# Kernel optimization log

Measured on AMD Instinct MI355X. Metric: run time of the kernel, lower is better.

The kernel has to match this reference:

```python
import jax, jax.numpy as jnp
import numpy as np

N_NODES = 50000
N_EDGES = 1600000
F_NODE, F_EDGE, HID = 16, 8, 64


def setup_inputs() -> dict:
    key = jax.random.key(0)
    ks = jax.random.split(key, 12)
    def w(k, shape):
        fan_in = shape[0]
        return jax.random.normal(k, shape, dtype=jnp.float32) / np.sqrt(fan_in)
    return {
        "x": jax.random.normal(ks[0], (N_NODES, F_NODE), dtype=jnp.float32),
        "edge_index": jax.random.randint(ks[1], (2, N_EDGES), 0, N_NODES, dtype=jnp.int32),
        "edge_attr": jax.random.normal(ks[2], (N_EDGES, F_EDGE), dtype=jnp.float32),
        "W1": w(ks[3], (F_NODE, HID)), "b1": jnp.zeros((HID,), jnp.float32),
        "W2": w(ks[4], (HID, HID)), "b2": jnp.zeros((HID,), jnp.float32),
        "mW1": w(ks[5], (2 * HID + F_EDGE, 2 * HID)), "mb1": jnp.zeros((2 * HID,), jnp.float32),
        "mW2": w(ks[6], (2 * HID, HID)), "mb2": jnp.zeros((HID,), jnp.float32),
        "mW3": w(ks[7], (HID, 1)), "mb3": jnp.zeros((1,), jnp.float32),
    }


def _gcn_conv(x, W, b, src, dst, deg_inv_sqrt, n_nodes):
    # GCNConv: D^{-1/2} (A + I) D^{-1/2} X W + b, edges include self-loops
    xw = x @ W  # [N, H]
    norm = deg_inv_sqrt[src] * deg_inv_sqrt[dst]  # [E+N]
    agg = jax.ops.segment_sum(xw[src] * norm[:, None], dst, num_segments=n_nodes)
    return agg + b


def reference(x, edge_index, edge_attr, W1, b1, W2, b2, mW1, mb1, mW2, mb2, mW3, mb3):
    n_nodes = x.shape[0]
    loop = jnp.arange(n_nodes, dtype=edge_index.dtype)
    src = jnp.concatenate([edge_index[0], loop])  # add self-loops
    dst = jnp.concatenate([edge_index[1], loop])
    deg = jax.ops.segment_sum(jnp.ones_like(dst, dtype=x.dtype), dst, num_segments=n_nodes)
    dis = jnp.where(deg > 0, jax.lax.rsqrt(deg), 0.0)

    h = jax.nn.relu(_gcn_conv(x, W1, b1, src, dst, dis, n_nodes))
    h = jax.nn.relu(_gcn_conv(h, W2, b2, src, dst, dis, n_nodes))

    # Vectorized equivalent of the per-graph neighbor loop: Q for every
    # (current_node=src, neighbor=dst) directed edge using its edge_attr.
    h_cur = h[edge_index[0]]   # [E, H]
    h_nbr = h[edge_index[1]]   # [E, H]
    z = jnp.concatenate([h_cur, h_nbr, edge_attr], axis=-1)  # [E, 2H+Fe]
    z = jax.nn.relu(z @ mW1 + mb1)
    z = jax.nn.relu(z @ mW2 + mb2)
    q = (z @ mW3 + mb3)[:, 0]  # [E]
    return q
```

## Files before the change

### kernel.cpp

```cpp
#include <hip/hip_runtime.h>
#include <hip/hip_bf16.h>

#define HID 64
#define FNODE 16
#define FEDGE 8
#define ZSTR 160

typedef __bf16 v8bf __attribute__((ext_vector_type(8)));
typedef unsigned short us8 __attribute__((ext_vector_type(8)));
typedef float v4f __attribute__((ext_vector_type(4)));

__device__ __bf16 g_w1h[20480];
__device__ __bf16 g_w1l[20480];
__device__ __bf16 g_w2h[8192];
__device__ __bf16 g_w2l[8192];

__global__ void k_pack(const float* __restrict__ mW1, const float* __restrict__ mW2) {
    int gid = blockIdx.x * 256 + threadIdx.x;
    if (gid < 20480) {
        int j = gid & 7, lane = (gid >> 3) & 63, f = gid >> 9;
        int kt = f >> 3, nt = f & 7;
        int k = kt * 32 + (lane >> 4) * 8 + j;
        int col = nt * 16 + (lane & 15);
        float x = (k < 136) ? mW1[k * 128 + col] : 0.f;
        __bf16 hi = (__bf16)x;
        g_w1h[gid] = hi;
        g_w1l[gid] = (__bf16)(x - (float)hi);
    } else if (gid < 28672) {
        int t = gid - 20480;
        int j = t & 7, lane = (t >> 3) & 63, f = t >> 9;
        int kt = f >> 2, nt = f & 3;
        int k = kt * 32 + (lane >> 4) * 8 + j;
        int col = nt * 16 + (lane & 15);
        float x = mW2[k * 64 + col];
        __bf16 hi = (__bf16)x;
        g_w2h[t] = hi;
        g_w2l[t] = (__bf16)(x - (float)hi);
    }
}

__global__ void k_count(const int* __restrict__ ei, int* __restrict__ rp, int E) {
    int e = blockIdx.x * 256 + threadIdx.x;
    if (e < E) atomicAdd(&rp[ei[E + e]], 1);
}

__global__ void k_disn(const int* __restrict__ rp, float* __restrict__ dis, int N) {
    int n = blockIdx.x * 256 + threadIdx.x;
    if (n < N) dis[n] = rsqrtf((float)(rp[n] + 1));
}

__device__ __forceinline__ int block_scan_excl(int v, int* wsum) {
    int lane = threadIdx.x & 63, wv = threadIdx.x >> 6;
    int inc = v;
#pragma unroll
    for (int d = 1; d < 64; d <<= 1) {
        int t = __shfl_up(inc, d, 64);
        if (lane >= d) inc += t;
    }
    if (lane == 63) wsum[wv] = inc;
    __syncthreads();
    int off = 0;
    for (int w = 0; w < wv; ++w) off += wsum[w];
    return off + inc - v;
}

__global__ void k_scan1(int* __restrict__ rp, int* __restrict__ bsum, int N) {
    __shared__ int ws[4];
    int i = blockIdx.x * 256 + threadIdx.x;
    int v = (i < N) ? rp[i] : 0;
    int excl = block_scan_excl(v, ws);
    if (i < N) rp[i] = excl;
    if (threadIdx.x == 255) bsum[blockIdx.x] = excl + v;
}

__global__ void k_scan2(int* __restrict__ bsum, int nb) {
    __shared__ int ws[4];
    int i = threadIdx.x;
    int v = (i < nb) ? bsum[i] : 0;
    int excl = block_scan_excl(v, ws);
    if (i < nb) bsum[i] = excl;
}

__global__ void k_scan3(int* __restrict__ rp, const int* __restrict__ bsum, int N) {
    int i = blockIdx.x * 256 + threadIdx.x;
    if (i < N) rp[i] += bsum[i >> 8];
}

__global__ void k_fill(const int* __restrict__ ei, int* __restrict__ rp,
                       int* __restrict__ ce, int* __restrict__ eid, int E) {
    int e = blockIdx.x * 256 + threadIdx.x;
    if (e < E) {
        int s = ei[e], d = ei[E + e];
        int pos = atomicAdd(&rp[d], 1);
        ce[pos] = s | (d << 16);
        eid[pos] = e;
    }
}

__global__ void k_dx(const float* __restrict__ x, const float* __restrict__ dis,
                     float* __restrict__ dx, int NF) {
    int t = blockIdx.x * 256 + threadIdx.x;
    if (t < NF) dx[t] = x[t] * dis[t >> 4];
}

__global__ __launch_bounds__(256) void k_pull1x(const float* __restrict__ dx,
                                                const int* __restrict__ rp,
                                                const int* __restrict__ ce,
                                                const float* __restrict__ dis,
                                                float* __restrict__ u, int N) {
    int grp = threadIdx.x >> 4, dim = threadIdx.x & 15;
    int n = blockIdx.x * 16 + grp;
    if (n >= N) return;
    int beg = n ? rp[n - 1] : 0;
    int end = rp[n];
    float a0 = dx[(size_t)n * 16 + dim];
    float a1 = 0.f, a2 = 0.f, a3 = 0.f;
    int j = beg;
    for (; j + 3 < end; j += 4) {
        int s0 = ce[j] & 0xffff, s1 = ce[j + 1] & 0xffff;
        int s2 = ce[j + 2] & 0xffff, s3 = ce[j + 3] & 0xffff;
        a0 += dx[(size_t)s0 * 16 + dim];
        a1 += dx[(size_t)s1 * 16 + dim];
        a2 += dx[(size_t)s2 * 16 + dim];
        a3 += dx[(size_t)s3 * 16 + dim];
    }
    for (; j < end; ++j) a0 += dx[(size_t)(ce[j] & 0xffff) * 16 + dim];
    u[(size_t)n * 16 + dim] = dis[n] * ((a0 + a1) + (a2 + a3));
}

__global__ __launch_bounds__(256) void k_h1y2(const float* __restrict__ u,
                                              const float* __restrict__ W1,
                                              const float* __restrict__ b1,
                                              const float* __restrict__ W2,
                                              const float* __restrict__ dis,
                                              float* __restrict__ y2, int N) {
    __shared__ float sh[4][64];
    int wave = threadIdx.x >> 6, lane = threadIdx.x & 63;
    int n = blockIdx.x * 4 + wave;
    if (n >= N) return;
    float myu = u[(size_t)n * 16 + (lane & 15)];
    float h = b1[lane];
#pragma unroll
    for (int k = 0; k < 16; ++k)
        h = fmaf(__shfl(myu, k, 64), W1[k * HID + lane], h);
    h = fmaxf(h, 0.f);
    sh[wave][lane] = h;
    float acc = 0.f;
#pragma unroll 8
    for (int k = 0; k < HID; ++k)
        acc = fmaf(sh[wave][k], W2[k * HID + lane], acc);
    y2[(size_t)n * HID + lane] = dis[n] * acc;
}

__global__ __launch_bounds__(256) void k_pull2(const float* __restrict__ y,
                                               const int* __restrict__ rp,
                                               const int* __restrict__ ce,
                                               const float* __restrict__ dis,
                                               const float* __restrict__ b,
                                               __bf16* __restrict__ hp, int N) {
    int wave = threadIdx.x >> 6, lane = threadIdx.x & 63;
    int n = blockIdx.x * 4 + wave;
    if (n >= N) return;
    int beg = n ? rp[n - 1] : 0;
    int end = rp[n];
    float a0 = y[(size_t)n * HID + lane];
    float a1 = 0.f, a2 = 0.f, a3 = 0.f;
    int j = beg;
    for (; j + 3 < end; j += 4) {
        int s0 = ce[j] & 0xffff, s1 = ce[j + 1] & 0xffff;
        int s2 = ce[j + 2] & 0xffff, s3 = ce[j + 3] & 0xffff;
        a0 += y[(size_t)s0 * HID + lane];
        a1 += y[(size_t)s1 * HID + lane];
        a2 += y[(size_t)s2 * HID + lane];
        a3 += y[(size_t)s3 * HID + lane];
    }
    for (; j < end; ++j) a0 += y[(size_t)(ce[j] & 0xffff) * HID + lane];
    float v = fmaxf(dis[n] * ((a0 + a1) + (a2 + a3)) + b[lane], 0.f);
    __bf16 hi = (__bf16)v;
    __bf16* p = hp + (size_t)n * 128;
    p[lane] = hi;
    p[64 + lane] = (__bf16)(v - (float)hi);
}

__global__ __launch_bounds__(256) void k_edge_mlp(
    const __bf16* __restrict__ hp, const int* __restrict__ ce,
    const int* __restrict__ eid, const float* __restrict__ ea,
    const float* __restrict__ mb1, const float* __restrict__ mb2,
    const float* __restrict__ mW3, const float* __restrict__ mb3,
    float* __restrict__ q, int E) {
    __shared__ __align__(16) __bf16 zh[64][ZSTR];
    __shared__ __align__(16) __bf16 zl[64][ZSTR];

    const int tid = threadIdx.x;
    const int lane = tid & 63;
    const int wave = tid >> 6;
    const int g = lane >> 4;
    const int cb = lane & 15;
    const int m0 = blockIdx.x * 64;

    {
        const int m = tid >> 2, qt = tid & 3;
        const int p = m0 + m;
        const bool valid = p < E;
        const int cep = valid ? ce[p] : 0;
        const int e = valid ? eid[p] : 0;
        const int s = cep & 0xffff;
        const int d = ((unsigned)cep) >> 16;
        const us8* S = (const us8*)(hp + (size_t)s * 128);
        const us8* D = (const us8*)(hp + (size_t)d * 128);
#pragma unroll
        for (int cc = 0; cc < 4; ++cc) {
            int c = qt * 4 + cc;
            us8 vs = S[c];
            us8 vd = D[c];
            __bf16* dst = (c < 8) ? &zh[m][0] : &zl[m][0];
            int base = (c & 7) * 8;
            *(us8*)&dst[base] = vs;
            *(us8*)&dst[64 + base] = vd;
        }
        if (qt < 2) {
            float buf[8];
#pragma unroll
            for (int i = 0; i < 8; ++i) buf[i] = valid ? ea[(size_t)e * FEDGE + i] : 0.f;
            __bf16* dst = qt ? &zl[m][0] : &zh[m][0];
            if (qt == 0) {
#pragma unroll
                for (int i = 0; i < 8; ++i) dst[128 + i] = (__bf16)buf[i];
            } else {
#pragma unroll
                for (int i = 0; i < 8; ++i) {
                    __bf16 h = (__bf16)buf[i];
                    dst[128 + i] = (__bf16)(buf[i] - (float)h);
                }
            }
            us8 zz = {};
#pragma unroll
            for (int c = 136; c < 160; c += 8) *(us8*)&dst[c] = zz;
        }
    }
    __syncthreads();

    const int nt0 = wave * 2;
    v4f acc[2][4];
    {
        float b0 = mb1[nt0 * 16 + cb];
        float b1v = mb1[nt0 * 16 + 16 + cb];
#pragma unroll
        for (int mt = 0; mt < 4; ++mt) {
            acc[0][mt] = (v4f){b0, b0, b0, b0};
            acc[1][mt] = (v4f){b1v, b1v, b1v, b1v};
        }
    }
    const v8bf* w1h = (const v8bf*)g_w1h;
    const v8bf* w1l = (const v8bf*)g_w1l;
#pragma unroll
    for (int kt = 0; kt < 5; ++kt) {
        v8bf bh0 = w1h[(kt * 8 + nt0) * 64 + lane];
        v8bf bl0 = w1l[(kt * 8 + nt0) * 64 + lane];
        v8bf bh1 = w1h[(kt * 8 + nt0 + 1) * 64 + lane];
        v8bf bl1 = w1l[(kt * 8 + nt0 + 1) * 64 + lane];
#pragma unroll
        for (int mt = 0; mt < 4; ++mt) {
            v8bf ah = *(const v8bf*)&zh[mt * 16 + cb][kt * 32 + g * 8];
            v8bf al = *(const v8bf*)&zl[mt * 16 + cb][kt * 32 + g * 8];
            acc[0][mt] = __builtin_amdgcn_mfma_f32_16x16x32_bf16(ah, bh0, acc[0][mt], 0, 0, 0);
            acc[0][mt] = __builtin_amdgcn_mfma_f32_16x16x32_bf16(ah, bl0, acc[0][mt], 0, 0, 0);
            acc[0][mt] = __builtin_amdgcn_mfma_f32_16x16x32_bf16(al, bh0, acc[0][mt], 0, 0, 0);
            acc[1][mt] = __builtin_amdgcn_mfma_f32_16x16x32_bf16(ah, bh1, acc[1][mt], 0, 0, 0);
            acc[1][mt] = __builtin_amdgcn_mfma_f32_16x16x32_bf16(ah, bl1, acc[1][mt], 0, 0, 0);
            acc[1][mt] = __builtin_amdgcn_mfma_f32_16x16x32_bf16(al, bh1, acc[1][mt], 0, 0, 0);
        }
    }
    __syncthreads();

#pragma unroll
    for (int c = 0; c < 2; ++c)
#pragma unroll
        for (int mt = 0; mt < 4; ++mt)
#pragma unroll
            for (int r = 0; r < 4; ++r) {
                float vv = fmaxf(acc[c][mt][r], 0.f);
                __bf16 hi = (__bf16)vv;
                int row = mt * 16 + g * 4 + r;
                int colx = (nt0 + c) * 16 + cb;
                zh[row][colx] = hi;
                zl[row][colx] = (__bf16)(vv - (float)hi);
            }
    __syncthreads();

    v4f acc2[4];
    {
        float b = mb2[wave * 16 + cb];
#pragma unroll
        for (int mt = 0; mt < 4; ++mt) acc2[mt] = (v4f){b, b, b, b};
    }
    const v8bf* w2h = (const v8bf*)g_w2h;
    const v8bf* w2l = (const v8bf*)g_w2l;
#pragma unroll
    for (int kt = 0; kt < 4; ++kt) {
        v8bf bh = w2h[(kt * 4 + wave) * 64 + lane];
        v8bf bl = w2l[(kt * 4 + wave) * 64 + lane];
#pragma unroll
        for (int mt = 0; mt < 4; ++mt) {
            v8bf ah = *(const v8bf*)&zh[mt * 16 + cb][kt * 32 + g * 8];
            v8bf al = *(const v8bf*)&zl[mt * 16 + cb][kt * 32 + g * 8];
            acc2[mt] = __builtin_amdgcn_mfma_f32_16x16x32_bf16(ah, bh, acc2[mt], 0, 0, 0);
            acc2[mt] = __builtin_amdgcn_mfma_f32_16x16x32_bf16(ah, bl, acc2[mt], 0, 0, 0);
            acc2[mt] = __builtin_amdgcn_mfma_f32_16x16x32_bf16(al, bh, acc2[mt], 0, 0, 0);
        }
    }
    __syncthreads();

    float* qp = (float*)&zh[0][0];
    const float w3 = mW3[wave * 16 + cb];
#pragma unroll
    for (int mt = 0; mt < 4; ++mt) {
#pragma unroll
        for (int r = 0; r < 4; ++r) {
            float pr = fmaxf(acc2[mt][r], 0.f) * w3;
            pr += __shfl_xor(pr, 1, 16);
            pr += __shfl_xor(pr, 2, 16);
            pr += __shfl_xor(pr, 4, 16);
            pr += __shfl_xor(pr, 8, 16);
            if (cb == 0) qp[wave * 64 + mt * 16 + g * 4 + r] = pr;
        }
    }
    __syncthreads();
    if (tid < 64) {
        int p = m0 + tid;
        if (p < E)
            q[eid[p]] = qp[tid] + qp[64 + tid] + qp[128 + tid] + qp[192 + tid] +
                        mb3[0];
    }
}

extern "C" void kernel_launch(void* const* d_in, const int* in_sizes, int n_in,
                              void* d_out, int out_size, void* d_ws, size_t ws_size,
                              hipStream_t stream) {
    const float* x   = (const float*)d_in[0];
    const int*   ei  = (const int*)d_in[1];
    const float* ea  = (const float*)d_in[2];
    const float* W1  = (const float*)d_in[3];
    const float* b1  = (const float*)d_in[4];
    const float* W2  = (const float*)d_in[5];
    const float* b2  = (const float*)d_in[6];
    const float* mW1 = (const float*)d_in[7];
    const float* mb1 = (const float*)d_in[8];
    const float* mW2 = (const float*)d_in[9];
    const float* mb2 = (const float*)d_in[10];
    const float* mW3 = (const float*)d_in[11];
    const float* mb3 = (const float*)d_in[12];
    float* q = (float*)d_out;

    const int N = in_sizes[0] / FNODE;
    const int E = in_sizes[1] / 2;

    float* dis = (float*)d_ws;
    int* bsum  = (int*)(dis + 50000);
    float* y2  = dis + ((N + 511) & ~255);
    float* hpf = y2 + (size_t)N * HID;
    float* dx  = hpf;
    float* u   = hpf + (size_t)N * 16;
    int* rp    = (int*)(hpf + (size_t)N * HID);
    int* ce    = rp + ((N + 255) & ~255);
    int* eid   = ce + E;

    const int nT = 256;
    const int gN    = (N + nT - 1) / nT;
    const int gE    = (E + nT - 1) / nT;
    const int gNF   = (N * FNODE + nT - 1) / nT;
    const int g16   = (N + 15) / 16;
    const int gNode = (N + 3) / 4;
    const int gMLP  = (E + 63) / 64;

    k_pack<<<112, nT, 0, stream>>>(mW1, mW2);

    hipMemsetAsync(rp, 0, (size_t)N * sizeof(int), stream);
    k_count<<<gE, nT, 0, stream>>>(ei, rp, E);
    k_disn<<<gN, nT, 0, stream>>>(rp, dis, N);
    k_scan1<<<gN, nT, 0, stream>>>(rp, bsum, N);
    k_scan2<<<1, nT, 0, stream>>>(bsum, gN);
    k_scan3<<<gN, nT, 0, stream>>>(rp, bsum, N);
    k_fill<<<gE, nT, 0, stream>>>(ei, rp, ce, eid, E);

    k_dx<<<gNF, nT, 0, stream>>>(x, dis, dx, N * FNODE);
    k_pull1x<<<g16, nT, 0, stream>>>(dx, rp, ce, dis, u, N);
    k_h1y2<<<gNode, nT, 0, stream>>>(u, W1, b1, W2, dis, y2, N);

    k_pull2<<<gNode, nT, 0, stream>>>(y2, rp, ce, dis, b2, (__bf16*)hpf, N);

    k_edge_mlp<<<gMLP, nT, 0, stream>>>((const __bf16*)hpf, ce, eid, ea, mb1, mb2,
                                        mW3, mb3, q, E);
}
```

Measured before the change: 757.3 us.

## Make edge MLP persistent with register-prefetched next tile; unroll gathers by eight

Turns the edge MLP kernel into a persistent grid-stride loop over 64-edge tiles on 1024 blocks. While the current tile is in the MFMA phases, the next tile's node features and edge attributes are gathered into registers to hide gather latency. The two GCN pull kernels also unroll their neighbor loops to eight independent accumulators for more loads in flight. The trade-off is higher register pressure from the prefetch buffers under the (256,4) launch bound, and a fixed grid size that may not match the device well.

```diff
diff --git a/kernel.cpp b/kernel.cpp
--- a/kernel.cpp
+++ b/kernel.cpp
@@ -114,18 +114,21 @@
     int beg = n ? rp[n - 1] : 0;
     int end = rp[n];
     float a0 = dx[(size_t)n * 16 + dim];
-    float a1 = 0.f, a2 = 0.f, a3 = 0.f;
+    float a1 = 0.f, a2 = 0.f, a3 = 0.f, a4 = 0.f, a5 = 0.f, a6 = 0.f, a7 = 0.f;
     int j = beg;
-    for (; j + 3 < end; j += 4) {
-        int s0 = ce[j] & 0xffff, s1 = ce[j + 1] & 0xffff;
-        int s2 = ce[j + 2] & 0xffff, s3 = ce[j + 3] & 0xffff;
-        a0 += dx[(size_t)s0 * 16 + dim];
-        a1 += dx[(size_t)s1 * 16 + dim];
-        a2 += dx[(size_t)s2 * 16 + dim];
-        a3 += dx[(size_t)s3 * 16 + dim];
+    for (; j + 7 < end; j += 8) {
+        a0 += dx[(size_t)(ce[j] & 0xffff) * 16 + dim];
+        a1 += dx[(size_t)(ce[j + 1] & 0xffff) * 16 + dim];
+        a2 += dx[(size_t)(ce[j + 2] & 0xffff) * 16 + dim];
+        a3 += dx[(size_t)(ce[j + 3] & 0xffff) * 16 + dim];
+        a4 += dx[(size_t)(ce[j + 4] & 0xffff) * 16 + dim];
+        a5 += dx[(size_t)(ce[j + 5] & 0xffff) * 16 + dim];
+        a6 += dx[(size_t)(ce[j + 6] & 0xffff) * 16 + dim];
+        a7 += dx[(size_t)(ce[j + 7] & 0xffff) * 16 + dim];
     }
     for (; j < end; ++j) a0 += dx[(size_t)(ce[j] & 0xffff) * 16 + dim];
-    u[(size_t)n * 16 + dim] = dis[n] * ((a0 + a1) + (a2 + a3));
+    u[(size_t)n * 16 + dim] =
+        dis[n] * (((a0 + a1) + (a2 + a3)) + ((a4 + a5) + (a6 + a7)));
 }
 
 __global__ __launch_bounds__(256) void k_h1y2(const float* __restrict__ u,
@@ -164,30 +167,39 @@
     int beg = n ? rp[n - 1] : 0;
     int end = rp[n];
     float a0 = y[(size_t)n * HID + lane];
-    float a1 = 0.f, a2 = 0.f, a3 = 0.f;
+    float a1 = 0.f, a2 = 0.f, a3 = 0.f, a4 = 0.f, a5 = 0.f, a6 = 0.f, a7 = 0.f;
     int j = beg;
-    for (; j + 3 < end; j += 4) {
-        int s0 = ce[j] & 0xffff, s1 = ce[j + 1] & 0xffff;
-        int s2 = ce[j + 2] & 0xffff, s3 = ce[j + 3] & 0xffff;
-        a0 += y[(size_t)s0 * HID + lane];
-        a1 += y[(size_t)s1 * HID + lane];
-        a2 += y[(size_t)s2 * HID + lane];
-        a3 += y[(size_t)s3 * HID + lane];
+    for (; j + 7 < end; j += 8) {
+        a0 += y[(size_t)(ce[j] & 0xffff) * HID + lane];
+        a1 += y[(size_t)(ce[j + 1] & 0xffff) * HID + lane];
+        a2 += y[(size_t)(ce[j + 2] & 0xffff) * HID + lane];
+        a3 += y[(size_t)(ce[j + 3] & 0xffff) * HID + lane];
+        a4 += y[(size_t)(ce[j + 4] & 0xffff) * HID + lane];
+        a5 += y[(size_t)(ce[j + 5] & 0xffff) * HID + lane];
+        a6 += y[(size_t)(ce[j + 6] & 0xffff) * HID + lane];
+        a7 += y[(size_t)(ce[j + 7] & 0xffff) * HID + lane];
     }
     for (; j < end; ++j) a0 += y[(size_t)(ce[j] & 0xffff) * HID + lane];
-    float v = fmaxf(dis[n] * ((a0 + a1) + (a2 + a3)) + b[lane], 0.f);
+    float v = fmaxf(
+        dis[n] * (((a0 + a1) + (a2 + a3)) + ((a4 + a5) + (a6 + a7))) + b[lane], 0.f);
     __bf16 hi = (__bf16)v;
     __bf16* p = hp + (size_t)n * 128;
     p[lane] = hi;
     p[64 + lane] = (__bf16)(v - (float)hi);
 }
 
-__global__ __launch_bounds__(256) void k_edge_mlp(
+struct ETile {
+    us8 s0, s1, s2, s3;
+    us8 d0, d1, d2, d3;
+    float4 ea;
+};
+
+__global__ __launch_bounds__(256, 4) void k_edge_mlp(
     const __bf16* __restrict__ hp, const int* __restrict__ ce,
     const int* __restrict__ eid, const float* __restrict__ ea,
     const float* __restrict__ mb1, const float* __restrict__ mb2,
     const float* __restrict__ mW3, const float* __restrict__ mb3,
-    float* __restrict__ q, int E) {
+    float* __restrict__ q, int E, int nTiles) {
     __shared__ __align__(16) __bf16 zh[64][ZSTR];
     __shared__ __align__(16) __bf16 zl[64][ZSTR];
 
@@ -196,141 +208,167 @@
     const int wave = tid >> 6;
     const int g = lane >> 4;
     const int cb = lane & 15;
-    const int m0 = blockIdx.x * 64;
-
-    {
-        const int m = tid >> 2, qt = tid & 3;
-        const int p = m0 + m;
-        const bool valid = p < E;
-        const int cep = valid ? ce[p] : 0;
-        const int e = valid ? eid[p] : 0;
-        const int s = cep & 0xffff;
-        const int d = ((unsigned)cep) >> 16;
-        const us8* S = (const us8*)(hp + (size_t)s * 128);
-        const us8* D = (const us8*)(hp + (size_t)d * 128);
-#pragma unroll
-        for (int cc = 0; cc < 4; ++cc) {
-            int c = qt * 4 + cc;
-            us8 vs = S[c];
-            us8 vd = D[c];
-            __bf16* dst = (c < 8) ? &zh[m][0] : &zl[m][0];
-            int base = (c & 7) * 8;
-            *(us8*)&dst[base] = vs;
-            *(us8*)&dst[64 + base] = vd;
-        }
-        if (qt < 2) {
-            float buf[8];
-#pragma unroll
-            for (int i = 0; i < 8; ++i) buf[i] = valid ? ea[(size_t)e * FEDGE + i] : 0.f;
-            __bf16* dst = qt ? &zl[m][0] : &zh[m][0];
-            if (qt == 0) {
-#pragma unroll
-                for (int i = 0; i < 8; ++i) dst[128 + i] = (__bf16)buf[i];
-            } else {
-#pragma unroll
-                for (int i = 0; i < 8; ++i) {
-                    __bf16 h = (__bf16)buf[i];
-                    dst[128 + i] = (__bf16)(buf[i] - (float)h);
-                }
-            }
-            us8 zz = {};
-#pragma unroll
-            for (int c = 136; c < 160; c += 8) *(us8*)&dst[c] = zz;
-        }
-    }
-    __syncthreads();
-
-    const int nt0 = wave * 2;
-    v4f acc[2][4];
-    {
-        float b0 = mb1[nt0 * 16 + cb];
-        float b1v = mb1[nt0 * 16 + 16 + cb];
-#pragma unroll
-        for (int mt = 0; mt < 4; ++mt) {
-            acc[0][mt] = (v4f){b0, b0, b0, b0};
-            acc[1][mt] = (v4f){b1v, b1v, b1v, b1v};
-        }
-    }
+    const int m = tid >> 2, qt = tid & 3;
+    const int stride = gridDim.x;
+
     const v8bf* w1h = (const v8bf*)g_w1h;
     const v8bf* w1l = (const v8bf*)g_w1l;
-#pragma unroll
-    for (int kt = 0; kt < 5; ++kt) {
-        v8bf bh0 = w1h[(kt * 8 + nt0) * 64 + lane];
-        v8bf bl0 = w1l[(kt * 8 + nt0) * 64 + lane];
-        v8bf bh1 = w1h[(kt * 8 + nt0 + 1) * 64 + lane];
-        v8bf bl1 = w1l[(kt * 8 + nt0 + 1) * 64 + lane];
-#pragma unroll
-        for (int mt = 0; mt < 4; ++mt) {
-            v8bf ah = *(const v8bf*)&zh[mt * 16 + cb][kt * 32 + g * 8];
-            v8bf al = *(const v8bf*)&zl[mt * 16 + cb][kt * 32 + g * 8];
-            acc[0][mt] = __builtin_amdgcn_mfma_f32_16x16x32_bf16(ah, bh0, acc[0][mt], 0, 0, 0);
-            acc[0][mt] = __builtin_amdgcn_mfma_f32_16x16x32_bf16(ah, bl0, acc[0][mt], 0, 0, 0);
-            acc[0][mt] = __builtin_amdgcn_mfma_f32_16x16x32_bf16(al, bh0, acc[0][mt], 0, 0, 0);
-            acc[1][mt] = __builtin_amdgcn_mfma_f32_16x16x32_bf16(ah, bh1, acc[1][mt], 0, 0, 0);
-            acc[1][mt] = __builtin_amdgcn_mfma_f32_16x16x32_bf16(ah, bl1, acc[1][mt], 0, 0, 0);
-            acc[1][mt] = __builtin_amdgcn_mfma_f32_16x16x32_bf16(al, bh1, acc[1][mt], 0, 0, 0);
-        }
-    }
-    __syncthreads();
-
-#pragma unroll
-    for (int c = 0; c < 2; ++c)
-#pragma unroll
-        for (int mt = 0; mt < 4; ++mt)
-#pragma unroll
-            for (int r = 0; r < 4; ++r) {
-                float vv = fmaxf(acc[c][mt][r], 0.f);
-                __bf16 hi = (__bf16)vv;
-                int row = mt * 16 + g * 4 + r;
-                int colx = (nt0 + c) * 16 + cb;
-                zh[row][colx] = hi;
-                zl[row][colx] = (__bf16)(vv - (float)hi);
-            }
-    __syncthreads();
-
-    v4f acc2[4];
-    {
-        float b = mb2[wave * 16 + cb];
-#pragma unroll
-        for (int mt = 0; mt < 4; ++mt) acc2[mt] = (v4f){b, b, b, b};
-    }
     const v8bf* w2h = (const v8bf*)g_w2h;
     const v8bf* w2l = (const v8bf*)g_w2l;
-#pragma unroll
-    for (int kt = 0; kt < 4; ++kt) {
-        v8bf bh = w2h[(kt * 4 + wave) * 64 + lane];
-        v8bf bl = w2l[(kt * 4 + wave) * 64 + lane];
+    const int nt0 = wave * 2;
+
+    auto prefetch = [&](int t, ETile& T) {
+        int p = t * 64 + m;
+        bool valid = p < E;
+        int cep = valid ? ce[p] : 0;
+        int s = cep & 0xffff;
+        int d = ((unsigned)cep) >> 16;
+        const us8* S = (const us8*)(hp + (size_t)s * 128) + qt * 4;
+        const us8* D = (const us8*)(hp + (size_t)d * 128) + qt * 4;
+        T.s0 = S[0]; T.s1 = S[1]; T.s2 = S[2]; T.s3 = S[3];
+        T.d0 = D[0]; T.d1 = D[1]; T.d2 = D[2]; T.d3 = D[3];
+        if (qt < 2) {
+            if (valid) {
+                int e = eid[p];
+                T.ea = *(const float4*)(ea + (size_t)e * FEDGE + qt * 4);
+            } else {
+                T.ea = (float4){0.f, 0.f, 0.f, 0.f};
+            }
+        }
+    };
+
+    auto stage = [&](const ETile& T) {
+#define PUTC(cc, VS, VD)                                     \
+    {                                                        \
+        int c = qt * 4 + cc;                                 \
+        __bf16* dst = (c < 8) ? &zh[m][0] : &zl[m][0];       \
+        int base = (c & 7) * 8;                              \
+        *(us8*)&dst[base] = VS;                              \
+        *(us8*)&dst[64 + base] = VD;                         \
+    }
+        PUTC(0, T.s0, T.d0)
+        PUTC(1, T.s1, T.d1)
+        PUTC(2, T.s2, T.d2)
+        PUTC(3, T.s3, T.d3)
+#undef PUTC
+        if (qt < 2) {
+            int base = 128 + qt * 4;
+#define PUTEA(i, V)                                  \
+    {                                                \
+        __bf16 hiv = (__bf16)(V);                    \
+        zh[m][base + i] = hiv;                       \
+        zl[m][base + i] = (__bf16)((V) - (float)hiv);\
+    }
+            PUTEA(0, T.ea.x) PUTEA(1, T.ea.y) PUTEA(2, T.ea.z) PUTEA(3, T.ea.w)
+#undef PUTEA
+        } else {
+            __bf16* dst = (qt == 2) ? &zh[m][136] : &zl[m][136];
+            us8 zz = {};
+            *(us8*)&dst[0] = zz;
+            *(us8*)&dst[8] = zz;
+            *(us8*)&dst[16] = zz;
+        }
+    };
+
+    ETile A, B;
+    int t = blockIdx.x;
+    if (t < nTiles) prefetch(t, A);
+
+    for (; t < nTiles; t += stride) {
+        __syncthreads();
+        stage(A);
+        int tn = t + stride;
+        if (tn < nTiles) prefetch(tn, B);
+        __syncthreads();
+
+        v4f acc[2][4];
+        {
+            float b0 = mb1[nt0 * 16 + cb];
+            float b1v = mb1[nt0 * 16 + 16 + cb];
+#pragma unroll
+            for (int mt = 0; mt < 4; ++mt) {
+                acc[0][mt] = (v4f){b0, b0, b0, b0};
+                acc[1][mt] = (v4f){b1v, b1v, b1v, b1v};
+            }
+        }
+#pragma unroll
+        for (int kt = 0; kt < 5; ++kt) {
+            v8bf bh0 = w1h[(kt * 8 + nt0) * 64 + lane];
+            v8bf bl0 = w1l[(kt * 8 + nt0) * 64 + lane];
+            v8bf bh1 = w1h[(kt * 8 + nt0 + 1) * 64 + lane];
+            v8bf bl1 = w1l[(kt * 8 + nt0 + 1) * 64 + lane];
+#pragma unroll
+            for (int mt = 0; mt < 4; ++mt) {
+                v8bf ah = *(const v8bf*)&zh[mt * 16 + cb][kt * 32 + g * 8];
+                v8bf al = *(const v8bf*)&zl[mt * 16 + cb][kt * 32 + g * 8];
+                acc[0][mt] = __builtin_amdgcn_mfma_f32_16x16x32_bf16(ah, bh0, acc[0][mt], 0, 0, 0);
+                acc[0][mt] = __builtin_amdgcn_mfma_f32_16x16x32_bf16(ah, bl0, acc[0][mt], 0, 0, 0);
+                acc[0][mt] = __builtin_amdgcn_mfma_f32_16x16x32_bf16(al, bh0, acc[0][mt], 0, 0, 0);
+                acc[1][mt] = __builtin_amdgcn_mfma_f32_16x16x32_bf16(ah, bh1, acc[1][mt], 0, 0, 0);
+                acc[1][mt] = __builtin_amdgcn_mfma_f32_16x16x32_bf16(ah, bl1, acc[1][mt], 0, 0, 0);
+                acc[1][mt] = __builtin_amdgcn_mfma_f32_16x16x32_bf16(al, bh1, acc[1][mt], 0, 0, 0);
+            }
+        }
+        __syncthreads();
+
+#pragma unroll
+        for (int c = 0; c < 2; ++c)
+#pragma unroll
+            for (int mt = 0; mt < 4; ++mt)
+#pragma unroll
+                for (int r = 0; r < 4; ++r) {
+                    float vv = fmaxf(acc[c][mt][r], 0.f);
+                    __bf16 hi = (__bf16)vv;
+                    int row = mt * 16 + g * 4 + r;
+                    int colx = (nt0 + c) * 16 + cb;
+                    zh[row][colx] = hi;
+                    zl[row][colx] = (__bf16)(vv - (float)hi);
+                }
+        __syncthreads();
+
+        v4f acc2[4];
+        {
+            float b = mb2[wave * 16 + cb];
+#pragma unroll
+            for (int mt = 0; mt < 4; ++mt) acc2[mt] = (v4f){b, b, b, b};
+        }
+#pragma unroll
+        for (int kt = 0; kt < 4; ++kt) {
+            v8bf bh = w2h[(kt * 4 + wave) * 64 + lane];
+            v8bf bl = w2l[(kt * 4 + wave) * 64 + lane];
+#pragma unroll
+            for (int mt = 0; mt < 4; ++mt) {
+                v8bf ah = *(const v8bf*)&zh[mt * 16 + cb][kt * 32 + g * 8];
+                v8bf al = *(const v8bf*)&zl[mt * 16 + cb][kt * 32 + g * 8];
+                acc2[mt] = __builtin_amdgcn_mfma_f32_16x16x32_bf16(ah, bh, acc2[mt], 0, 0, 0);
+                acc2[mt] = __builtin_amdgcn_mfma_f32_16x16x32_bf16(ah, bl, acc2[mt], 0, 0, 0);
+                acc2[mt] = __builtin_amdgcn_mfma_f32_16x16x32_bf16(al, bh, acc2[mt], 0, 0, 0);
+            }
+        }
+        __syncthreads();
+
+        float* qp = (float*)&zh[0][0];
+        const float w3 = mW3[wave * 16 + cb];
 #pragma unroll
         for (int mt = 0; mt < 4; ++mt) {
-            v8bf ah = *(const v8bf*)&zh[mt * 16 + cb][kt * 32 + g * 8];
-            v8bf al = *(const v8bf*)&zl[mt * 16 + cb][kt * 32 + g * 8];
-            acc2[mt] = __builtin_amdgcn_mfma_f32_16x16x32_bf16(ah, bh, acc2[mt], 0, 0, 0);
-            acc2[mt] = __builtin_amdgcn_mfma_f32_16x16x32_bf16(ah, bl, acc2[mt], 0, 0, 0);
-            acc2[mt] = __builtin_amdgcn_mfma_f32_16x16x32_bf16(al, bh, acc2[mt], 0, 0, 0);
-        }
-    }
-    __syncthreads();
-
-    float* qp = (float*)&zh[0][0];
-    const float w3 = mW3[wave * 16 + cb];
-#pragma unroll
-    for (int mt = 0; mt < 4; ++mt) {
-#pragma unroll
-        for (int r = 0; r < 4; ++r) {
-            float pr = fmaxf(acc2[mt][r], 0.f) * w3;
-            pr += __shfl_xor(pr, 1, 16);
-            pr += __shfl_xor(pr, 2, 16);
-            pr += __shfl_xor(pr, 4, 16);
-            pr += __shfl_xor(pr, 8, 16);
-            if (cb == 0) qp[wave * 64 + mt * 16 + g * 4 + r] = pr;
-        }
-    }
-    __syncthreads();
-    if (tid < 64) {
-        int p = m0 + tid;
-        if (p < E)
-            q[eid[p]] = qp[tid] + qp[64 + tid] + qp[128 + tid] + qp[192 + tid] +
-                        mb3[0];
+#pragma unroll
+            for (int r = 0; r < 4; ++r) {
+                float pr = fmaxf(acc2[mt][r], 0.f) * w3;
+                pr += __shfl_xor(pr, 1, 16);
+                pr += __shfl_xor(pr, 2, 16);
+                pr += __shfl_xor(pr, 4, 16);
+                pr += __shfl_xor(pr, 8, 16);
+                if (cb == 0) qp[wave * 64 + mt * 16 + g * 4 + r] = pr;
+            }
+        }
+        __syncthreads();
+        if (tid < 64) {
+            int p = t * 64 + tid;
+            if (p < E)
+                q[eid[p]] =
+                    qp[tid] + qp[64 + tid] + qp[128 + tid] + qp[192 + tid] + mb3[0];
+        }
+        A = B;
     }
 }
 
@@ -371,7 +409,7 @@
     const int gNF   = (N * FNODE + nT - 1) / nT;
     const int g16   = (N + 15) / 16;
     const int gNode = (N + 3) / 4;
-    const int gMLP  = (E + 63) / 64;
+    const int nTiles = (E + 63) / 64;
 
     k_pack<<<112, nT, 0, stream>>>(mW1, mW2);
 
@@ -389,6 +427,6 @@
 
     k_pull2<<<gNode, nT, 0, stream>>>(y2, rp, ce, dis, b2, (__bf16*)hpf, N);
 
-    k_edge_mlp<<<gMLP, nT, 0, stream>>>((const __bf16*)hpf, ce, eid, ea, mb1, mb2,
-                                        mW3, mb3, q, E);
-}
+    k_edge_mlp<<<1024, nT, 0, stream>>>((const __bf16*)hpf, ce, eid, ea, mb1, mb2,
+                                        mW3, mb3, q, E, nTiles);
+}
```

Result: slower. 951.5 us (+25.6%).

## Gather node features straight to LDS and retile edge-MLP staging layout

Applied to the files above, without the earlier changes.

The edge MLP now gathers the source and destination node rows with global_load_lds (direct global-to-LDS DMA) into a new tiled LDS layout given by zoff. Edge attributes go into separate small hi/lo buffers loaded as float4. The goal is to skip the register round trip and cut LDS bank conflicts in the A-operand reads. The two pull kernels also unroll the neighbour gather from 4 to 8 accumulators for more memory-level parallelism. This adds complex layout indexing and relies on the exact byte layout of the LDS DMA, where a mismatch would corrupt data.

```diff
diff --git a/kernel.cpp b/kernel.cpp
--- a/kernel.cpp
+++ b/kernel.cpp
@@ -4,7 +4,6 @@
 #define HID 64
 #define FNODE 16
 #define FEDGE 8
-#define ZSTR 160
 
 typedef __bf16 v8bf __attribute__((ext_vector_type(8)));
 typedef unsigned short us8 __attribute__((ext_vector_type(8)));
@@ -114,18 +113,21 @@
     int beg = n ? rp[n - 1] : 0;
     int end = rp[n];
     float a0 = dx[(size_t)n * 16 + dim];
-    float a1 = 0.f, a2 = 0.f, a3 = 0.f;
+    float a1 = 0.f, a2 = 0.f, a3 = 0.f, a4 = 0.f, a5 = 0.f, a6 = 0.f, a7 = 0.f;
     int j = beg;
-    for (; j + 3 < end; j += 4) {
-        int s0 = ce[j] & 0xffff, s1 = ce[j + 1] & 0xffff;
-        int s2 = ce[j + 2] & 0xffff, s3 = ce[j + 3] & 0xffff;
-        a0 += dx[(size_t)s0 * 16 + dim];
-        a1 += dx[(size_t)s1 * 16 + dim];
-        a2 += dx[(size_t)s2 * 16 + dim];
-        a3 += dx[(size_t)s3 * 16 + dim];
+    for (; j + 7 < end; j += 8) {
+        a0 += dx[(size_t)(ce[j] & 0xffff) * 16 + dim];
+        a1 += dx[(size_t)(ce[j + 1] & 0xffff) * 16 + dim];
+        a2 += dx[(size_t)(ce[j + 2] & 0xffff) * 16 + dim];
+        a3 += dx[(size_t)(ce[j + 3] & 0xffff) * 16 + dim];
+        a4 += dx[(size_t)(ce[j + 4] & 0xffff) * 16 + dim];
+        a5 += dx[(size_t)(ce[j + 5] & 0xffff) * 16 + dim];
+        a6 += dx[(size_t)(ce[j + 6] & 0xffff) * 16 + dim];
+        a7 += dx[(size_t)(ce[j + 7] & 0xffff) * 16 + dim];
     }
     for (; j < end; ++j) a0 += dx[(size_t)(ce[j] & 0xffff) * 16 + dim];
-    u[(size_t)n * 16 + dim] = dis[n] * ((a0 + a1) + (a2 + a3));
+    u[(size_t)n * 16 + dim] =
+        dis[n] * (((a0 + a1) + (a2 + a3)) + ((a4 + a5) + (a6 + a7)));
 }
 
 __global__ __launch_bounds__(256) void k_h1y2(const float* __restrict__ u,
@@ -164,22 +166,29 @@
     int beg = n ? rp[n - 1] : 0;
     int end = rp[n];
     float a0 = y[(size_t)n * HID + lane];
-    float a1 = 0.f, a2 = 0.f, a3 = 0.f;
+    float a1 = 0.f, a2 = 0.f, a3 = 0.f, a4 = 0.f, a5 = 0.f, a6 = 0.f, a7 = 0.f;
     int j = beg;
-    for (; j + 3 < end; j += 4) {
-        int s0 = ce[j] & 0xffff, s1 = ce[j + 1] & 0xffff;
-        int s2 = ce[j + 2] & 0xffff, s3 = ce[j + 3] & 0xffff;
-        a0 += y[(size_t)s0 * HID + lane];
-        a1 += y[(size_t)s1 * HID + lane];
-        a2 += y[(size_t)s2 * HID + lane];
-        a3 += y[(size_t)s3 * HID + lane];
+    for (; j + 7 < end; j += 8) {
+        a0 += y[(size_t)(ce[j] & 0xffff) * HID + lane];
+        a1 += y[(size_t)(ce[j + 1] & 0xffff) * HID + lane];
+        a2 += y[(size_t)(ce[j + 2] & 0xffff) * HID + lane];
+        a3 += y[(size_t)(ce[j + 3] & 0xffff) * HID + lane];
+        a4 += y[(size_t)(ce[j + 4] & 0xffff) * HID + lane];
+        a5 += y[(size_t)(ce[j + 5] & 0xffff) * HID + lane];
+        a6 += y[(size_t)(ce[j + 6] & 0xffff) * HID + lane];
+        a7 += y[(size_t)(ce[j + 7] & 0xffff) * HID + lane];
     }
     for (; j < end; ++j) a0 += y[(size_t)(ce[j] & 0xffff) * HID + lane];
-    float v = fmaxf(dis[n] * ((a0 + a1) + (a2 + a3)) + b[lane], 0.f);
+    float v = fmaxf(
+        dis[n] * (((a0 + a1) + (a2 + a3)) + ((a4 + a5) + (a6 + a7))) + b[lane], 0.f);
     __bf16 hi = (__bf16)v;
     __bf16* p = hp + (size_t)n * 128;
     p[lane] = hi;
     p[64 + lane] = (__bf16)(v - (float)hi);
+}
+
+__device__ __forceinline__ int zoff(int m, int ch) {
+    return ((m >> 4) << 12) + ((ch >> 2) << 9) + ((m & 15) << 5) + ((ch & 3) << 3);
 }
 
 __global__ __launch_bounds__(256) void k_edge_mlp(
@@ -188,8 +197,9 @@
     const float* __restrict__ mb1, const float* __restrict__ mb2,
     const float* __restrict__ mW3, const float* __restrict__ mb3,
     float* __restrict__ q, int E) {
-    __shared__ __align__(16) __bf16 zh[64][ZSTR];
-    __shared__ __align__(16) __bf16 zl[64][ZSTR];
+    __shared__ __align__(16) __bf16 zc[16384];
+    __shared__ __align__(16) __bf16 eh[64][32];
+    __shared__ __align__(16) __bf16 el[64][32];
 
     const int tid = threadIdx.x;
     const int lane = tid & 63;
@@ -199,43 +209,53 @@
     const int m0 = blockIdx.x * 64;
 
     {
+        const int me = wave * 16 + (lane >> 2);
+        const int cl = lane & 3;
+        const int p = m0 + me;
+        const bool valid = p < E;
+        const int cep = valid ? ce[p] : 0;
+        const int s = cep & 0xffff;
+        const int d = ((unsigned)cep) >> 16;
+        const __bf16* Sp = hp + (size_t)s * 128 + cl * 8;
+        const __bf16* Dp = hp + (size_t)d * 128 + cl * 8;
+        __bf16* lb = zc + wave * 4096;
+#pragma unroll
+        for (int i = 0; i < 4; ++i)
+            __builtin_amdgcn_global_load_lds(
+                (const __attribute__((address_space(1))) unsigned int*)(Sp + i * 32),
+                (__attribute__((address_space(3))) unsigned int*)(lb + i * 512),
+                16, 0, 0);
+#pragma unroll
+        for (int i = 0; i < 4; ++i)
+            __builtin_amdgcn_global_load_lds(
+                (const __attribute__((address_space(1))) unsigned int*)(Dp + i * 32),
+                (__attribute__((address_space(3))) unsigned int*)(lb + (4 + i) * 512),
+                16, 0, 0);
+    }
+    {
         const int m = tid >> 2, qt = tid & 3;
         const int p = m0 + m;
         const bool valid = p < E;
-        const int cep = valid ? ce[p] : 0;
-        const int e = valid ? eid[p] : 0;
-        const int s = cep & 0xffff;
-        const int d = ((unsigned)cep) >> 16;
-        const us8* S = (const us8*)(hp + (size_t)s * 128);
-        const us8* D = (const us8*)(hp + (size_t)d * 128);
-#pragma unroll
-        for (int cc = 0; cc < 4; ++cc) {
-            int c = qt * 4 + cc;
-            us8 vs = S[c];
-            us8 vd = D[c];
-            __bf16* dst = (c < 8) ? &zh[m][0] : &zl[m][0];
-            int base = (c & 7) * 8;
-            *(us8*)&dst[base] = vs;
-            *(us8*)&dst[64 + base] = vd;
-        }
         if (qt < 2) {
-            float buf[8];
-#pragma unroll
-            for (int i = 0; i < 8; ++i) buf[i] = valid ? ea[(size_t)e * FEDGE + i] : 0.f;
-            __bf16* dst = qt ? &zl[m][0] : &zh[m][0];
-            if (qt == 0) {
-#pragma unroll
-                for (int i = 0; i < 8; ++i) dst[128 + i] = (__bf16)buf[i];
-            } else {
-#pragma unroll
-                for (int i = 0; i < 8; ++i) {
-                    __bf16 h = (__bf16)buf[i];
-                    dst[128 + i] = (__bf16)(buf[i] - (float)h);
-                }
+            float4 v = {0.f, 0.f, 0.f, 0.f};
+            if (valid) {
+                int e = eid[p];
+                v = *(const float4*)(ea + (size_t)e * FEDGE + qt * 4);
             }
+            const float* vf = (const float*)&v;
+#pragma unroll
+            for (int i2 = 0; i2 < 4; ++i2) {
+                float vv = vf[i2];
+                __bf16 hiv = (__bf16)vv;
+                eh[m][qt * 4 + i2] = hiv;
+                el[m][qt * 4 + i2] = (__bf16)(vv - (float)hiv);
+            }
+        } else {
             us8 zz = {};
-#pragma unroll
-            for (int c = 136; c < 160; c += 8) *(us8*)&dst[c] = zz;
+            __bf16* dstp = (qt == 2) ? &eh[m][8] : &el[m][8];
+            *(us8*)&dstp[0] = zz;
+            *(us8*)&dstp[8] = zz;
+            *(us8*)&dstp[16] = zz;
         }
     }
     __syncthreads();
@@ -253,6 +273,8 @@
     }
     const v8bf* w1h = (const v8bf*)g_w1h;
     const v8bf* w1l = (const v8bf*)g_w1l;
+    const v8bf* w2h = (const v8bf*)g_w2h;
+    const v8bf* w2l = (const v8bf*)g_w2l;
 #pragma unroll
     for (int kt = 0; kt < 5; ++kt) {
         v8bf bh0 = w1h[(kt * 8 + nt0) * 64 + lane];
@@ -261,8 +283,15 @@
         v8bf bl1 = w1l[(kt * 8 + nt0 + 1) * 64 + lane];
 #pragma unroll
         for (int mt = 0; mt < 4; ++mt) {
-            v8bf ah = *(const v8bf*)&zh[mt * 16 + cb][kt * 32 + g * 8];
-            v8bf al = *(const v8bf*)&zl[mt * 16 + cb][kt * 32 + g * 8];
+            v8bf ah, al;
+            if (kt < 4) {
+                int ch = (kt < 2) ? kt * 4 + g : 16 + (kt - 2) * 4 + g;
+                ah = *(const v8bf*)&zc[zoff(mt * 16 + cb, ch)];
+                al = *(const v8bf*)&zc[zoff(mt * 16 + cb, ch + 8)];
+            } else {
+                ah = *(const v8bf*)&eh[mt * 16 + cb][g * 8];
+                al = *(const v8bf*)&el[mt * 16 + cb][g * 8];
+            }
             acc[0][mt] = __builtin_amdgcn_mfma_f32_16x16x32_bf16(ah, bh0, acc[0][mt], 0, 0, 0);
             acc[0][mt] = __builtin_amdgcn_mfma_f32_16x16x32_bf16(ah, bl0, acc[0][mt], 0, 0, 0);
             acc[0][mt] = __builtin_amdgcn_mfma_f32_16x16x32_bf16(al, bh0, acc[0][mt], 0, 0, 0);
@@ -280,11 +309,12 @@
 #pragma unroll
             for (int r = 0; r < 4; ++r) {
                 float vv = fmaxf(acc[c][mt][r], 0.f);
-                __bf16 hi = (__bf16)vv;
+                __bf16 hiv = (__bf16)vv;
                 int row = mt * 16 + g * 4 + r;
-                int colx = (nt0 + c) * 16 + cb;
-                zh[row][colx] = hi;
-                zl[row][colx] = (__bf16)(vv - (float)hi);
+                int col = (nt0 + c) * 16 + cb;
+                int chh = (col < 64) ? (col >> 3) : (8 + (col >> 3));
+                zc[zoff(row, chh) + (cb & 7)] = hiv;
+                zc[zoff(row, chh + 8) + (cb & 7)] = (__bf16)(vv - (float)hiv);
             }
     __syncthreads();
 
@@ -294,16 +324,15 @@
 #pragma unroll
         for (int mt = 0; mt < 4; ++mt) acc2[mt] = (v4f){b, b, b, b};
     }
-    const v8bf* w2h = (const v8bf*)g_w2h;
-    const v8bf* w2l = (const v8bf*)g_w2l;
 #pragma unroll
     for (int kt = 0; kt < 4; ++kt) {
         v8bf bh = w2h[(kt * 4 + wave) * 64 + lane];
         v8bf bl = w2l[(kt * 4 + wave) * 64 + lane];
+        int ch = (kt < 2) ? kt * 4 + g : 16 + (kt - 2) * 4 + g;
 #pragma unroll
         for (int mt = 0; mt < 4; ++mt) {
-            v8bf ah = *(const v8bf*)&zh[mt * 16 + cb][kt * 32 + g * 8];
-            v8bf al = *(const v8bf*)&zl[mt * 16 + cb][kt * 32 + g * 8];
+            v8bf ah = *(const v8bf*)&zc[zoff(mt * 16 + cb, ch)];
+            v8bf al = *(const v8bf*)&zc[zoff(mt * 16 + cb, ch + 8)];
             acc2[mt] = __builtin_amdgcn_mfma_f32_16x16x32_bf16(ah, bh, acc2[mt], 0, 0, 0);
             acc2[mt] = __builtin_amdgcn_mfma_f32_16x16x32_bf16(ah, bl, acc2[mt], 0, 0, 0);
             acc2[mt] = __builtin_amdgcn_mfma_f32_16x16x32_bf16(al, bh, acc2[mt], 0, 0, 0);
@@ -311,7 +340,7 @@
     }
     __syncthreads();
 
-    float* qp = (float*)&zh[0][0];
+    float* qp = (float*)&zc[0];
     const float w3 = mW3[wave * 16 + cb];
 #pragma unroll
     for (int mt = 0; mt < 4; ++mt) {
@@ -329,8 +358,8 @@
     if (tid < 64) {
         int p = m0 + tid;
         if (p < E)
-            q[eid[p]] = qp[tid] + qp[64 + tid] + qp[128 + tid] + qp[192 + tid] +
-                        mb3[0];
+            q[eid[p]] =
+                qp[tid] + qp[64 + tid] + qp[128 + tid] + qp[192 + tid] + mb3[0];
     }
 }
 
```

Result: faster. 713.6 us (-5.8%).
